# Performance work log

Hardware: AMD Instinct MI355X
Metric: run time of the kernel (lower is better)

Reference implementation:

```python
import jax, jax.numpy as jnp
import numpy as np

B, L = 16, 512          # samples x tokens-per-sample
S = B * L               # total packed tokens
H, HKV, D = 16, 4, 128  # query heads, kv heads, head_dim
G = H // HKV            # GQA group size
HID = 2048
EPS = 1e-6


def rmsnorm(x, w):
    # Qwen2RMSNorm: fp32 variance, scale by weight
    v = jnp.mean(x.astype(jnp.float32) ** 2, axis=-1, keepdims=True)
    return (x.astype(jnp.float32) * jax.lax.rsqrt(v + EPS)).astype(x.dtype) * w


def rotate_half(x):
    x1, x2 = jnp.split(x, 2, axis=-1)
    return jnp.concatenate([-x2, x1], axis=-1)


def setup_inputs() -> dict:
    key = jax.random.key(0)
    ks = jax.random.split(key, 24)
    f = lambda k, shp, s=0.02: (jax.random.normal(k, shp, dtype=jnp.float32) * s)
    inp = {
        'packed_sequence_und': f(ks[0], (S // 2, HID), 1.0),
        'packed_sequence_gen': f(ks[1], (S // 2, HID), 1.0),
        # und tokens on even slots, gen on odd slots -> irregular scatter
        'packed_und_token_indexes': jnp.arange(0, S, 2, dtype=jnp.int32),
        'packed_gen_token_indexes': jnp.arange(1, S, 2, dtype=jnp.int32),
        # und-path projections (q/k/v have bias, o does not)
        'q_w': f(ks[2], (H * D, HID)), 'q_b': f(ks[3], (H * D,)),
        'k_w': f(ks[4], (HKV * D, HID)), 'k_b': f(ks[5], (HKV * D,)),
        'v_w': f(ks[6], (HKV * D, HID)), 'v_b': f(ks[7], (HKV * D,)),
        'o_w': f(ks[8], (HID, H * D)),
        # gen-path (moe_gen) projections
        'q_w_g': f(ks[9], (H * D, HID)), 'q_b_g': f(ks[10], (H * D,)),
        'k_w_g': f(ks[11], (HKV * D, HID)), 'k_b_g': f(ks[12], (HKV * D,)),
        'v_w_g': f(ks[13], (HKV * D, HID)), 'v_b_g': f(ks[14], (HKV * D,)),
        'o_w_g': f(ks[15], (HID, H * D)),
        # qk-norm weights
        'qn_w': jnp.ones((D,), jnp.float32), 'kn_w': jnp.ones((D,), jnp.float32),
        'qn_w_g': jnp.ones((D,), jnp.float32), 'kn_w_g': jnp.ones((D,), jnp.float32),
    }
    # RoPE cos/sin for packed positions (position resets per sample)
    pos = jnp.tile(jnp.arange(L, dtype=jnp.float32), B)            # [S]
    inv_freq = 1.0 / (1e6 ** (jnp.arange(0, D, 2, dtype=jnp.float32) / D))
    freqs = pos[:, None] * inv_freq[None, :]                       # [S, D/2]
    emb = jnp.concatenate([freqs, freqs], axis=-1)                 # [S, D]
    inp['packed_cos'] = jnp.cos(emb)
    inp['packed_sin'] = jnp.sin(emb)
    return inp


def reference(packed_sequence_und, packed_sequence_gen, packed_cos, packed_sin,
              packed_und_token_indexes, packed_gen_token_indexes,
              q_w, q_b, k_w, k_b, v_w, v_b, o_w,
              q_w_g, q_b_g, k_w_g, k_b_g, v_w_g, v_b_g, o_w_g,
              qn_w, kn_w, qn_w_g, kn_w_g):
    ui, gi = packed_und_token_indexes, packed_gen_token_indexes
    # dual-path QKV projection + index scatter into shared packed buffers
    q = jnp.zeros((S, H * D), jnp.float32)
    q = q.at[ui].set(packed_sequence_und @ q_w.T + q_b)
    q = q.at[gi].set(packed_sequence_gen @ q_w_g.T + q_b_g)
    k = jnp.zeros((S, HKV * D), jnp.float32)
    k = k.at[ui].set(packed_sequence_und @ k_w.T + k_b)
    k = k.at[gi].set(packed_sequence_gen @ k_w_g.T + k_b_g)
    v = jnp.zeros((S, HKV * D), jnp.float32)
    v = v.at[ui].set(packed_sequence_und @ v_w.T + v_b)
    v = v.at[gi].set(packed_sequence_gen @ v_w_g.T + v_b_g)

    q = q.reshape(S, H, D)
    k = k.reshape(S, HKV, D)
    v = v.reshape(S, HKV, D)

    # per-stream QK RMSNorm, scattered back
    q = jnp.zeros_like(q).at[ui].set(rmsnorm(q[ui], qn_w)).at[gi].set(rmsnorm(q[gi], qn_w_g))
    k = jnp.zeros_like(k).at[ui].set(rmsnorm(k[ui], kn_w)).at[gi].set(rmsnorm(k[gi], kn_w_g))

    # RoPE (unsqueeze_dim=1)
    cos, sin = packed_cos[:, None, :], packed_sin[:, None, :]
    q = q * cos + rotate_half(q) * sin
    k = k * cos + rotate_half(k) * sin

    # block-diagonal causal attention over packed samples (GQA)
    qb_ = q.reshape(B, L, HKV, G, D)
    kb_ = k.reshape(B, L, HKV, D)
    vb_ = v.reshape(B, L, HKV, D)
    scale = 1.0 / np.sqrt(D)
    scores = jnp.einsum('bqhgd,bkhd->bhgqk', qb_, kb_) * scale   # [B,HKV,G,L,L]
    causal = jnp.tril(jnp.ones((L, L), bool))
    scores = jnp.where(causal, scores, -jnp.inf)
    probs = jax.nn.softmax(scores, axis=-1)
    out = jnp.einsum('bhgqk,bkhd->bqhgd', probs, vb_)            # [B,L,HKV,G,D]
    out = out.reshape(S, H * D)

    out_und = out[ui] @ o_w.T
    out_gen = out[gi] @ o_w_g.T
    return (out_und, out_gen)
```

## Files before the change

### kernel.cpp

```cpp
#include <hip/hip_runtime.h>

typedef __bf16 bf16;
typedef __bf16 bf16x8 __attribute__((ext_vector_type(8)));
typedef float  f32x4  __attribute__((ext_vector_type(4)));

#define HALF   4096
#define S_TOT  8192
#define HID    2048
#define NH     16
#define NKV    4
#define DH     128
#define LSEQ   512

typedef const __attribute__((address_space(1))) void* as1_cvp;
typedef __attribute__((address_space(3))) void* as3_vp;

__device__ __forceinline__ void gl2lds16(const void* g, void* l) {
    __builtin_amdgcn_global_load_lds((as1_cvp)g, (as3_vp)l, 16, 0, 0);
}

#define VMCNT(n) asm volatile("s_waitcnt vmcnt(" #n ")" ::: "memory")

struct CvtArgs {
    const float* src[10];
    bf16*        dst[10];
    int          n4[10];
};
__global__ __launch_bounds__(256) void k_convert_seg(CvtArgs a) {
    int rem = blockIdx.x;
    const float* src; bf16* dst;
    if      (rem < 8192)           { src=a.src[0]; dst=a.dst[0]; }
    else if ((rem -= 8192) < 8192) { src=a.src[1]; dst=a.dst[1]; }
    else if ((rem -= 8192) < 4096) { src=a.src[2]; dst=a.dst[2]; }
    else if ((rem -= 4096) < 1024) { src=a.src[3]; dst=a.dst[3]; }
    else if ((rem -= 1024) < 1024) { src=a.src[4]; dst=a.dst[4]; }
    else if ((rem -= 1024) < 4096) { src=a.src[5]; dst=a.dst[5]; }
    else if ((rem -= 4096) < 1024) { src=a.src[6]; dst=a.dst[6]; }
    else if ((rem -= 1024) < 1024) { src=a.src[7]; dst=a.dst[7]; }
    else if ((rem -= 1024) < 4096) { src=a.src[8]; dst=a.dst[8]; }
    else    { rem -= 4096;           src=a.src[9]; dst=a.dst[9]; }
    const int i = (rem << 8) + threadIdx.x;
    float4 v = ((const float4*)src)[i];
    union { bf16 b[4]; ushort4 u; } t;
    t.b[0] = (bf16)v.x; t.b[1] = (bf16)v.y; t.b[2] = (bf16)v.z; t.b[3] = (bf16)v.w;
    ((ushort4*)dst)[i] = t.u;
}

__global__ void k_invtyp(const int* __restrict__ ui, const int* __restrict__ gi,
                         int* __restrict__ it) {
    int t = blockIdx.x * 256 + threadIdx.x;
    if (t < HALF) { it[ui[t]] = t << 1; it[gi[t]] = (t << 1) | 1; }
}

__global__ __launch_bounds__(256) void k_gemm_qkv(
    const bf16* __restrict__ Xu, const bf16* __restrict__ Xg,
    const bf16* __restrict__ Wu, const bf16* __restrict__ Wg,
    const float* __restrict__ qbu, const float* __restrict__ kbu, const float* __restrict__ vbu,
    const float* __restrict__ qbg, const float* __restrict__ kbg, const float* __restrict__ vbg,
    const int* __restrict__ ui, const int* __restrict__ gi,
    bf16* __restrict__ qo, bf16* __restrict__ ko, bf16* __restrict__ vo)
{
    const int gen = blockIdx.z;
    const bf16* X = gen ? Xg : Xu;
    const bf16* W = gen ? Wg : Wu;
    const float* qb = gen ? qbg : qbu;
    const float* kb = gen ? kbg : kbu;
    const float* vb = gen ? vbg : vbu;
    const int* idx = gen ? gi : ui;

    __shared__ __align__(16) bf16 sA[128*32];
    __shared__ __align__(16) bf16 sB[128*32];

    const int tid = threadIdx.x;
    const int wave = tid >> 6, lane = tid & 63;
    const int lm = lane & 15, kq = lane >> 4;
    const int wm = wave >> 1, wn = wave & 1;
    const int m0 = blockIdx.y * 128, n0 = blockIdx.x * 128;

    f32x4 acc[4][4] = {};

    for (int k0 = 0; k0 < HID; k0 += 32) {
        __syncthreads();
        #pragma unroll
        for (int i = 0; i < 2; ++i) {
            const int g = i*4 + wave;
            const int c = g*64 + lane;
            const int row = c >> 2, col = c & 3;
            gl2lds16(X + (size_t)(m0+row)*HID + k0 + col*8, (char*)sA + (size_t)g*1024);
            gl2lds16(W + (size_t)(n0+row)*HID + k0 + col*8, (char*)sB + (size_t)g*1024);
        }
        __syncthreads();
        bf16x8 a[4], b[4];
        #pragma unroll
        for (int i = 0; i < 4; ++i) a[i] = *(const bf16x8*)&sA[(wm*64 + i*16 + lm)*32 + kq*8];
        #pragma unroll
        for (int j = 0; j < 4; ++j) b[j] = *(const bf16x8*)&sB[(wn*64 + j*16 + lm)*32 + kq*8];
        #pragma unroll
        for (int i = 0; i < 4; ++i)
            #pragma unroll
            for (int j = 0; j < 4; ++j)
                acc[i][j] = __builtin_amdgcn_mfma_f32_16x16x32_bf16(a[i], b[j], acc[i][j], 0, 0, 0);
    }

    #pragma unroll
    for (int i = 0; i < 4; ++i) {
        int srow[4];
        #pragma unroll
        for (int r = 0; r < 4; ++r) srow[r] = idx[m0 + wm*64 + i*16 + kq*4 + r];
        #pragma unroll
        for (int j = 0; j < 4; ++j) {
            const int o = n0 + wn*64 + j*16 + lm;
            bf16* dst; float bias; int off0, ld;
            if (o < 2048)      { dst = qo; ld = 2048; off0 = o;        bias = qb[o]; }
            else if (o < 2560) { dst = ko; ld = 512;  off0 = o - 2048; bias = kb[o-2048]; }
            else               { dst = vo; ld = 512;  off0 = o - 2560; bias = vb[o-2560]; }
            #pragma unroll
            for (int r = 0; r < 4; ++r)
                dst[(size_t)srow[r]*ld + off0] = (bf16)(acc[i][j][r] + bias);
        }
    }
}

#define C0 0
#define C1 16384
#define C2 32768
#define C3 49152

#define STG2(MB, KC, DST)                                                       \
    gl2lds16((MB) + (KC) + go0, (DST) + wave*1024);                             \
    gl2lds16((MB) + (KC) + go1, (DST) + 8192 + wave*1024);

#define PH(RD, MH, DOB, STG, TAIL)                                              \
  {                                                                             \
    _Pragma("unroll")                                                           \
    for (int im = 0; im < 4; ++im)                                              \
        a_[im] = *(const bf16x8*)(sAb + (RD) + (MH)*4096 + im*1024 + abase);    \
    if (DOB) {                                                                  \
        _Pragma("unroll")                                                       \
        for (int jn = 0; jn < 4; ++jn)                                          \
            b_[jn] = *(const bf16x8*)(sBb + (RD) + jn*1024 + bbase);            \
    }                                                                           \
    STG;                                                                        \
    __builtin_amdgcn_s_barrier();                                               \
    __builtin_amdgcn_s_setprio(1);                                              \
    _Pragma("unroll")                                                           \
    for (int im = 0; im < 4; ++im)                                              \
      _Pragma("unroll")                                                         \
      for (int jn = 0; jn < 4; ++jn)                                            \
        acc[(MH)*4+im][jn] = __builtin_amdgcn_mfma_f32_16x16x32_bf16(           \
            a_[im], b_[jn], acc[(MH)*4+im][jn], 0, 0, 0);                       \
    __builtin_amdgcn_s_setprio(0);                                              \
    TAIL;                                                                       \
    __builtin_amdgcn_s_barrier();                                               \
  }

__device__ __forceinline__ void gemm256_core(
    const bf16* __restrict__ A, const bf16* __restrict__ B,
    int m0, int n0, int tid, char* sAb, char* sBb, f32x4 (&acc)[8][4])
{
    const int lane = tid & 63;
    const int lm = lane & 15, kq = lane >> 4;
    const int wave = tid >> 6;
    const int wm = wave >> 2, wn = wave & 3;

    const int swz16 = (kq ^ ((lm >> 1) & 3)) * 16;
    const int abase = wm*8192 + lm*64 + swz16;
    const int bbase = wn*4096 + lm*64 + swz16;

    int go0, go1;
    {
        const int s0 = tid,        r0 = s0 >> 2, c0 = (s0 & 3) ^ ((r0 >> 1) & 3);
        const int s1 = 512 + tid,  r1 = s1 >> 2, c1 = (s1 & 3) ^ ((r1 >> 1) & 3);
        go0 = r0*HID + c0*8;
        go1 = r1*HID + c1*8;
    }
    const bf16* Ab = A + (size_t)m0*HID;
    const bf16* Bb = B + (size_t)n0*HID;

    bf16x8 a_[4], b_[4];

    STG2(Ab, 0,  sAb + C0);  STG2(Ab, 32, sAb + C1);
    STG2(Bb, 0,  sBb + C0);  STG2(Bb, 32, sBb + C1);
    STG2(Ab, 64, sAb + C2);  STG2(Bb, 64, sBb + C2);
    VMCNT(4);
    __builtin_amdgcn_s_barrier();

    #pragma unroll 1
    for (int i = 0; i < 15; ++i) {
        const int kc = 128*i;
        PH(C0, 0, 1, STG2(Ab, kc+96,  sAb+C3), (void)0);
        PH(C0, 1, 0, STG2(Bb, kc+96,  sBb+C3), (void)0);
        PH(C1, 0, 1, STG2(Ab, kc+128, sAb+C0), (void)0);
        PH(C1, 1, 0, STG2(Bb, kc+128, sBb+C0), VMCNT(4));
        PH(C2, 0, 1, STG2(Ab, kc+160, sAb+C1), (void)0);
        PH(C2, 1, 0, STG2(Bb, kc+160, sBb+C1), (void)0);
        PH(C3, 0, 1, STG2(Ab, kc+192, sAb+C2), (void)0);
        PH(C3, 1, 0, STG2(Bb, kc+192, sBb+C2), VMCNT(4));
    }
    {
        PH(C0, 0, 1, STG2(Ab, 2016, sAb+C3), (void)0);
        PH(C0, 1, 0, STG2(Bb, 2016, sBb+C3), (void)0);
        PH(C1, 0, 1, (void)0, (void)0);
        PH(C1, 1, 0, (void)0, VMCNT(0));
        PH(C2, 0, 1, (void)0, (void)0);
        PH(C2, 1, 0, (void)0, (void)0);
        PH(C3, 0, 1, (void)0, (void)0);
        PH(C3, 1, 0, (void)0, (void)0);
    }
}

__global__ __launch_bounds__(256) void k_norm_rope(
    bf16* __restrict__ qbuf, bf16* __restrict__ kbuf,
    const float* __restrict__ cosb, const float* __restrict__ sinb,
    const int* __restrict__ invtyp,
    const float* __restrict__ qnu, const float* __restrict__ qng,
    const float* __restrict__ knu, const float* __restrict__ kng)
{
    const int row = blockIdx.x * 4 + (threadIdx.x >> 6);
    const int lane = threadIdx.x & 63;
    const int s = row / (NH + NKV), hh = row % (NH + NKV);
    const int isg = invtyp[s] & 1;
    bf16* ptr; const float* w; float qs;
    if (hh < NH) { ptr = qbuf + (size_t)s*HID + hh*DH;           w = isg ? qng : qnu;
                   qs = 0.08838834764831845f * 1.4426950408889634f; }
    else         { ptr = kbuf + (size_t)s*(NKV*DH) + (hh-NH)*DH; w = isg ? kng : knu;
                   qs = 1.0f; }

    const unsigned u = *(const unsigned*)((const unsigned short*)ptr + 2*lane);
    const float f0 = __uint_as_float(u << 16);
    const float f1 = __uint_as_float(u & 0xffff0000u);
    float ss = f0*f0 + f1*f1;
    #pragma unroll
    for (int m = 32; m; m >>= 1) ss += __shfl_xor(ss, m, 64);
    const float r = rsqrtf(ss * (1.0f/128.0f) + 1e-6f);
    const float2 wv = *(const float2*)(w + 2*lane);
    const float xn0 = f0 * r * wv.x;
    const float xn1 = f1 * r * wv.y;
    const float po0 = __shfl_xor(xn0, 32, 64);
    const float po1 = __shfl_xor(xn1, 32, 64);
    const float2 c2 = *(const float2*)(cosb + (size_t)s*DH + 2*lane);
    const float2 s2 = *(const float2*)(sinb + (size_t)s*DH + 2*lane);
    const float sg = (lane < 32) ? -1.0f : 1.0f;
    const float o0 = (xn0 * c2.x + sg * po0 * s2.x) * qs;
    const float o1 = (xn1 * c2.y + sg * po1 * s2.y) * qs;
    union { unsigned short us[2]; unsigned u; } t;
    bf16 b0 = (bf16)o0, b1 = (bf16)o1;
    t.us[0] = *(unsigned short*)&b0; t.us[1] = *(unsigned short*)&b1;
    *(unsigned*)((unsigned short*)ptr + 2*lane) = t.u;
}

__global__ __launch_bounds__(256) void k_vtrans(const bf16* __restrict__ v, bf16* __restrict__ vt)
{
    __shared__ __align__(16) bf16 sT[64 * 132];
    const int kvh = blockIdx.y;
    const int s0 = blockIdx.x * 64;
    const int b = s0 >> 9;
    const int pos0 = s0 & 511;
    const int tid = threadIdx.x;

    #pragma unroll
    for (int i = 0; i < 4; ++i) {
        const int c = i*256 + tid;
        const int rowi = c >> 4, col8 = c & 15;
        const uint4 d = *(const uint4*)(v + (size_t)(s0 + rowi)*(NKV*DH) + kvh*DH + col8*8);
        uint2* lp = (uint2*)&sT[rowi*132 + col8*8];
        lp[0] = make_uint2(d.x, d.y);
        lp[1] = make_uint2(d.z, d.w);
    }
    __syncthreads();
    const int dd = tid >> 1, half = tid & 1;
    __align__(16) bf16 tmp[32];
    #pragma unroll
    for (int p = 0; p < 32; ++p) tmp[p] = sT[(half*32 + p)*132 + dd];
    bf16* dst = vt + ((size_t)(b*NKV + kvh)*DH + dd)*LSEQ + pos0 + half*32;
    #pragma unroll
    for (int q = 0; q < 8; ++q) ((ushort4*)dst)[q] = ((ushort4*)tmp)[q];
}

__global__ __launch_bounds__(256) void k_attn(
    const bf16* __restrict__ qbuf, const bf16* __restrict__ kbuf,
    const bf16* __restrict__ vt, const int* __restrict__ invtyp,
    bf16* __restrict__ aop_u, bf16* __restrict__ aop_g)
{
    __shared__ __align__(16) bf16 sK[2][64*128];
    __shared__ __align__(16) bf16 sV[2][128*64];
    __shared__ __align__(16) bf16 sP[4][16*72];

    const int pr = blockIdx.x;
    const int h = blockIdx.y, b = blockIdx.z;
    const int kvh = h >> 2;
    const int tid = threadIdx.x, wave = tid >> 6, lane = tid & 63;
    const int lm = lane & 15, kq = lane >> 4;

    const bf16* kbase = kbuf + ((size_t)(b*LSEQ))*(NKV*DH) + kvh*DH;
    const bf16* vbase = vt + ((size_t)(b*NKV + kvh)*DH)*LSEQ;
    bf16* const sPw = &sP[wave][0];

    #pragma unroll 1
    for (int t = 0; t < 2; ++t) {
        const int qt = t ? pr : 7 - pr;
        const int q0 = qt * 64;

        bf16x8 qfrag[4];
        {
            const bf16* qp = qbuf + ((size_t)(b*LSEQ + q0 + wave*16 + lm))*HID + h*DH;
            #pragma unroll
            for (int ks = 0; ks < 4; ++ks)
                qfrag[ks] = *(const bf16x8*)(qp + ks*32 + kq*8);
        }

        f32x4 accO[8] = {};
        float lpart[4] = {0.f, 0.f, 0.f, 0.f};

        if (t) __syncthreads();

        {
            const bf16* kp = kbase;
            const bf16* vp = vbase;
            #pragma unroll
            for (int i = 0; i < 4; ++i) {
                const int g = i*4 + wave;
                const int ch = g*64 + lane;
                { const int row = ch >> 4, cp = ch & 15;
                  const int c = (cp & 8) | ((cp ^ row) & 7);
                  gl2lds16(kp + (size_t)row*(NKV*DH) + c*8, (char*)&sK[0][0] + (size_t)g*1024); }
                { const int d = ch >> 3, cp = ch & 7;
                  const int c = (cp ^ d) & 7;
                  gl2lds16(vp + (size_t)d*LSEQ + c*8, (char*)&sV[0][0] + (size_t)g*1024); }
            }
        }

        for (int kt = 0; kt <= qt; ++kt) {
            const int cur = kt & 1;
            __syncthreads();

            if (kt < qt) {
                const bf16* kp = kbase + (size_t)((kt+1)*64)*(NKV*DH);
                const bf16* vp = vbase + (kt+1)*64;
                const int nxt = cur ^ 1;
                #pragma unroll
                for (int i = 0; i < 4; ++i) {
                    const int g = i*4 + wave;
                    const int ch = g*64 + lane;
                    { const int row = ch >> 4, cp = ch & 15;
                      const int c = (cp & 8) | ((cp ^ row) & 7);
                      gl2lds16(kp + (size_t)row*(NKV*DH) + c*8, (char*)&sK[nxt][0] + (size_t)g*1024); }
                    { const int d = ch >> 3, cp = ch & 7;
                      const int c = (cp ^ d) & 7;
                      gl2lds16(vp + (size_t)d*LSEQ + c*8, (char*)&sV[nxt][0] + (size_t)g*1024); }
                }
            }

            f32x4 s4[4] = {};
            #pragma unroll
            for (int ks = 0; ks < 4; ++ks) {
                const int cq = ks*4 + kq;
                const int cs = (cq & 8) | ((cq ^ lm) & 7);
                #pragma unroll
                for (int nt = 0; nt < 4; ++nt) {
                    bf16x8 bk = *(const bf16x8*)&sK[cur][(nt*16 + lm)*128 + cs*8];
                    s4[nt] = __builtin_amdgcn_mfma_f32_16x16x32_bf16(qfrag[ks], bk, s4[nt], 0, 0, 0);
                }
            }

            const bool diag = (kt == qt);
            #pragma unroll
            for (int r = 0; r < 4; ++r) {
                const int rloc = wave*16 + kq*4 + r;
                float v0 = s4[0][r], v1 = s4[1][r], v2 = s4[2][r], v3 = s4[3][r];
                if (diag) {
                    if (lm      > rloc) v0 = -1e30f;
                    if (lm + 16 > rloc) v1 = -1e30f;
                    if (lm + 32 > rloc) v2 = -1e30f;
                    if (lm + 48 > rloc) v3 = -1e30f;
                }
                const float p0 = exp2f(v0);
                const float p1 = exp2f(v1);
                const float p2 = exp2f(v2);
                const float p3 = exp2f(v3);
                lpart[r] += (p0 + p1) + (p2 + p3);
                const int prow = (kq*4 + r) * 72;
                sPw[prow + lm]      = (bf16)p0;
                sPw[prow + 16 + lm] = (bf16)p1;
                sPw[prow + 32 + lm] = (bf16)p2;
                sPw[prow + 48 + lm] = (bf16)p3;
            }

            #pragma unroll
            for (int pc = 0; pc < 2; ++pc) {
                bf16x8 ap = *(const bf16x8*)&sPw[lm*72 + pc*32 + kq*8];
                #pragma unroll
                for (int dt = 0; dt < 8; ++dt) {
                    const int cv = (pc*4 + kq);
                    const int cs = (cv ^ lm) & 7;
                    bf16x8 bv = *(const bf16x8*)&sV[cur][(dt*16 + lm)*64 + cs*8];
                    accO[dt] = __builtin_amdgcn_mfma_f32_16x16x32_bf16(ap, bv, accO[dt], 0, 0, 0);
                }
            }
        }

        #pragma unroll
        for (int r = 0; r < 4; ++r) {
            float l = lpart[r];
            l += __shfl_xor(l, 1, 64);
            l += __shfl_xor(l, 2, 64);
            l += __shfl_xor(l, 4, 64);
            l += __shfl_xor(l, 8, 64);
            const int srow = b*LSEQ + q0 + wave*16 + kq*4 + r;
            const int code = invtyp[srow];
            bf16* dst = (code & 1) ? aop_g : aop_u;
            const size_t off = (size_t)(code >> 1)*HID + h*DH;
            const float inv_l = 1.0f / l;
            #pragma unroll
            for (int dt = 0; dt < 8; ++dt)
                dst[off + dt*16 + lm] = (bf16)(accO[dt][r] * inv_l);
        }
    }
}

__global__ __launch_bounds__(512, 2) void k_gemm_out(
    const bf16* __restrict__ Au, const bf16* __restrict__ Ag,
    const bf16* __restrict__ Wu, const bf16* __restrict__ Wg,
    float* __restrict__ out)
{
    __shared__ __align__(16) bf16 sA[4][256*32];
    __shared__ __align__(16) bf16 sB[4][256*32];

    const int lin = blockIdx.x;
    const int idx = (lin & 7) * 32 + (lin >> 3);
    const int gen = idx / 128;
    const int rem = idx - gen * 128;
    const int my  = rem >> 3;
    const int nx_ = rem & 7;
    const int m0 = my * 256, n0 = nx_ * 256;

    const bf16* A = gen ? Ag : Au;
    const bf16* W = gen ? Wg : Wu;
    float* O = out + (size_t)gen * HALF * HID;

    const int tid = threadIdx.x;
    const int wave = tid >> 6, lane = tid & 63;
    const int lm = lane & 15, kq = lane >> 4;
    const int wm = wave >> 2, wn = wave & 3;

    f32x4 acc[8][4] = {};
    gemm256_core(A, W, m0, n0, tid, (char*)&sA[0][0], (char*)&sB[0][0], acc);

    #pragma unroll
    for (int im = 0; im < 8; ++im)
        #pragma unroll
        for (int jn = 0; jn < 4; ++jn)
            #pragma unroll
            for (int r = 0; r < 4; ++r)
                O[(size_t)(m0 + wm*128 + im*16 + kq*4 + r)*HID + (n0 + wn*64 + jn*16 + lm)]
                    = acc[im][jn][r];
}

extern "C" void kernel_launch(void* const* d_in, const int* in_sizes, int n_in,
                              void* d_out, int out_size, void* d_ws, size_t ws_size,
                              hipStream_t stream)
{
    (void)in_sizes; (void)n_in; (void)out_size; (void)ws_size;
    const float* x_u  = (const float*)d_in[0];
    const float* x_g  = (const float*)d_in[1];
    const int*   ui   = (const int*)d_in[2];
    const int*   gi   = (const int*)d_in[3];
    const float* q_w  = (const float*)d_in[4];
    const float* q_b  = (const float*)d_in[5];
    const float* k_w  = (const float*)d_in[6];
    const float* k_b  = (const float*)d_in[7];
    const float* v_w  = (const float*)d_in[8];
    const float* v_b  = (const float*)d_in[9];
    const float* o_w  = (const float*)d_in[10];
    const float* q_wg = (const float*)d_in[11];
    const float* q_bg = (const float*)d_in[12];
    const float* k_wg = (const float*)d_in[13];
    const float* k_bg = (const float*)d_in[14];
    const float* v_wg = (const float*)d_in[15];
    const float* v_bg = (const float*)d_in[16];
    const float* o_wg = (const float*)d_in[17];
    const float* qn_u = (const float*)d_in[18];
    const float* kn_u = (const float*)d_in[19];
    const float* qn_g = (const float*)d_in[20];
    const float* kn_g = (const float*)d_in[21];
    const float* cosb = (const float*)d_in[22];
    const float* sinb = (const float*)d_in[23];

    char* w = (char*)d_ws;
    auto alloc = [&](size_t bytes) { char* p = w; w += (bytes + 255) & ~(size_t)255; return p; };
    bf16* xb_u   = (bf16*)alloc((size_t)HALF*HID*2);
    bf16* xb_g   = (bf16*)alloc((size_t)HALF*HID*2);
    bf16* wqkv_u = (bf16*)alloc((size_t)3072*HID*2);
    bf16* wqkv_g = (bf16*)alloc((size_t)3072*HID*2);
    bf16* wo_u   = (bf16*)alloc((size_t)HID*HID*2);
    bf16* wo_g   = (bf16*)alloc((size_t)HID*HID*2);
    bf16* qbuf   = (bf16*)alloc((size_t)S_TOT*HID*2);
    bf16* kbuf   = (bf16*)alloc((size_t)S_TOT*NKV*DH*2);
    bf16* vbuf   = (bf16*)alloc((size_t)S_TOT*NKV*DH*2);
    bf16* vtb    = (bf16*)alloc((size_t)S_TOT*NKV*DH*2);
    int*  invtyp = (int*)alloc((size_t)S_TOT*4);
    bf16* aop_u = xb_u;
    bf16* aop_g = xb_g;

    CvtArgs ca;
    int si = 0;
    auto seg = [&](const float* s, bf16* d, size_t n) {
        ca.src[si] = s; ca.dst[si] = d; ca.n4[si] = (int)(n / 4); ++si;
    };
    seg(x_u,  xb_u,                (size_t)HALF*HID);
    seg(x_g,  xb_g,                (size_t)HALF*HID);
    seg(q_w,  wqkv_u,              (size_t)2048*HID);
    seg(k_w,  wqkv_u + 2048*HID,   (size_t)512*HID);
    seg(v_w,  wqkv_u + 2560*HID,   (size_t)512*HID);
    seg(q_wg, wqkv_g,              (size_t)2048*HID);
    seg(k_wg, wqkv_g + 2048*HID,   (size_t)512*HID);
    seg(v_wg, wqkv_g + 2560*HID,   (size_t)512*HID);
    seg(o_w,  wo_u,                (size_t)HID*HID);
    seg(o_wg, wo_g,                (size_t)HID*HID);
    k_convert_seg<<<36864, 256, 0, stream>>>(ca);

    k_invtyp<<<16, 256, 0, stream>>>(ui, gi, invtyp);

    k_gemm_qkv<<<dim3(24, 32, 2), 256, 0, stream>>>(
        xb_u, xb_g, wqkv_u, wqkv_g,
        q_b, k_b, v_b, q_bg, k_bg, v_bg,
        ui, gi, qbuf, kbuf, vbuf);

    k_norm_rope<<<(S_TOT*(NH+NKV))/4, 256, 0, stream>>>(
        qbuf, kbuf, cosb, sinb, invtyp, qn_u, qn_g, kn_u, kn_g);

    k_vtrans<<<dim3(S_TOT/64, NKV), 256, 0, stream>>>(vbuf, vtb);

    k_attn<<<dim3(4, NH, 16), 256, 0, stream>>>(
        qbuf, kbuf, vtb, invtyp, aop_u, aop_g);

    k_gemm_out<<<dim3(256), 512, 0, stream>>>(
        aop_u, aop_g, wo_u, wo_g, (float*)d_out);
}
```

Measured before the change: 504.9 us.

## Fuse QK RMSNorm and RoPE into QKV GEMM epilogue, merge invtyp into convert

The QKV projection epilogue now stages each 128-column head tile in shared memory, computes the per-row RMSNorm and RoPE there, and writes the final Q/K directly, so the separate norm/rope kernel and its read-modify-write pass over Q/K are gone. V tiles keep the plain bias-add scatter. The inverse-index kernel is folded into extra blocks of the convert launch, which saves one launch. In exchange the GEMM uses about 33KB more LDS, which may reduce occupancy, and the epilogue gains a barrier plus shuffle traffic.

```diff
diff --git a/kernel.cpp b/kernel.cpp
--- a/kernel.cpp
+++ b/kernel.cpp
@@ -21,13 +21,22 @@
 
 #define VMCNT(n) asm volatile("s_waitcnt vmcnt(" #n ")" ::: "memory")
 
+__device__ __forceinline__ float bfu_lo(unsigned u) { return __uint_as_float(u << 16); }
+__device__ __forceinline__ float bfu_hi(unsigned u) { return __uint_as_float(u & 0xffff0000u); }
+
 struct CvtArgs {
     const float* src[10];
     bf16*        dst[10];
     int          n4[10];
 };
-__global__ __launch_bounds__(256) void k_convert_seg(CvtArgs a) {
+__global__ __launch_bounds__(256) void k_convert_seg(CvtArgs a,
+    const int* __restrict__ ui, const int* __restrict__ gi, int* __restrict__ it) {
     int rem = blockIdx.x;
+    if (rem >= 36864) {
+        int t = (rem - 36864) * 256 + threadIdx.x;
+        if (t < HALF) { it[ui[t]] = t << 1; it[gi[t]] = (t << 1) | 1; }
+        return;
+    }
     const float* src; bf16* dst;
     if      (rem < 8192)           { src=a.src[0]; dst=a.dst[0]; }
     else if ((rem -= 8192) < 8192) { src=a.src[1]; dst=a.dst[1]; }
@@ -46,18 +55,15 @@
     ((ushort4*)dst)[i] = t.u;
 }
 
-__global__ void k_invtyp(const int* __restrict__ ui, const int* __restrict__ gi,
-                         int* __restrict__ it) {
-    int t = blockIdx.x * 256 + threadIdx.x;
-    if (t < HALF) { it[ui[t]] = t << 1; it[gi[t]] = (t << 1) | 1; }
-}
-
 __global__ __launch_bounds__(256) void k_gemm_qkv(
     const bf16* __restrict__ Xu, const bf16* __restrict__ Xg,
     const bf16* __restrict__ Wu, const bf16* __restrict__ Wg,
     const float* __restrict__ qbu, const float* __restrict__ kbu, const float* __restrict__ vbu,
     const float* __restrict__ qbg, const float* __restrict__ kbg, const float* __restrict__ vbg,
     const int* __restrict__ ui, const int* __restrict__ gi,
+    const float* __restrict__ qnu, const float* __restrict__ qng,
+    const float* __restrict__ knu, const float* __restrict__ kng,
+    const float* __restrict__ cosb, const float* __restrict__ sinb,
     bf16* __restrict__ qo, bf16* __restrict__ ko, bf16* __restrict__ vo)
 {
     const int gen = blockIdx.z;
@@ -70,6 +76,7 @@
 
     __shared__ __align__(16) bf16 sA[128*32];
     __shared__ __align__(16) bf16 sB[128*32];
+    __shared__ __align__(8)  bf16 sX[128*132];
 
     const int tid = threadIdx.x;
     const int wave = tid >> 6, lane = tid & 63;
@@ -102,21 +109,93 @@
                 acc[i][j] = __builtin_amdgcn_mfma_f32_16x16x32_bf16(a[i], b[j], acc[i][j], 0, 0, 0);
     }
 
+    const int nb = n0 >> 7;
+    if (nb >= 20) {
+        #pragma unroll
+        for (int i = 0; i < 4; ++i) {
+            int srow[4];
+            #pragma unroll
+            for (int r = 0; r < 4; ++r) srow[r] = idx[m0 + wm*64 + i*16 + kq*4 + r];
+            #pragma unroll
+            for (int j = 0; j < 4; ++j) {
+                const int o = n0 + wn*64 + j*16 + lm - 2560;
+                const float bias = vb[o];
+                #pragma unroll
+                for (int r = 0; r < 4; ++r)
+                    vo[(size_t)srow[r]*512 + o] = (bf16)(acc[i][j][r] + bias);
+            }
+        }
+        return;
+    }
+
+    const bool isQ = nb < 16;
+    const float* bptr = isQ ? (qb + n0) : (kb + (n0 - 2048));
+    const float* wnp  = isQ ? (gen ? qng : qnu) : (gen ? kng : knu);
+    bf16* obuf = isQ ? qo : ko;
+    const int old_ = isQ ? 2048 : 512;
+    const int ocol = (isQ ? nb : nb - 16) * 128;
+    const float qs = isQ ? (0.08838834764831845f * 1.4426950408889634f) : 1.0f;
+    char* const sXb = (char*)sX;
+
     #pragma unroll
-    for (int i = 0; i < 4; ++i) {
-        int srow[4];
-        #pragma unroll
-        for (int r = 0; r < 4; ++r) srow[r] = idx[m0 + wm*64 + i*16 + kq*4 + r];
+    for (int i = 0; i < 4; ++i)
         #pragma unroll
         for (int j = 0; j < 4; ++j) {
-            const int o = n0 + wn*64 + j*16 + lm;
-            bf16* dst; float bias; int off0, ld;
-            if (o < 2048)      { dst = qo; ld = 2048; off0 = o;        bias = qb[o]; }
-            else if (o < 2560) { dst = ko; ld = 512;  off0 = o - 2048; bias = kb[o-2048]; }
-            else               { dst = vo; ld = 512;  off0 = o - 2560; bias = vb[o-2560]; }
-            #pragma unroll
-            for (int r = 0; r < 4; ++r)
-                dst[(size_t)srow[r]*ld + off0] = (bf16)(acc[i][j][r] + bias);
+            const int d = wn*64 + j*16 + lm;
+            const float bias = bptr[d];
+            #pragma unroll
+            for (int r = 0; r < 4; ++r) {
+                bf16 xb = (bf16)(acc[i][j][r] + bias);
+                int us = (int)*(unsigned short*)&xb;
+                int pp = (us & 0xffff) | (__shfl_xor(us, 1, 64) << 16);
+                if (!(lm & 1)) {
+                    const int row = wm*64 + i*16 + kq*4 + r;
+                    *(unsigned*)(sXb + row*264 + d*2) = (unsigned)pp;
+                }
+            }
+        }
+    __syncthreads();
+
+    {
+        const int row = tid >> 1, hf = tid & 1;
+        const int srow = idx[m0 + row];
+        const char* rp = sXb + row*264;
+
+        float ss = 0.f;
+        #pragma unroll
+        for (int c = 0; c < 16; ++c) {
+            uint2 u2 = *(const uint2*)(rp + hf*128 + c*8);
+            float f0 = bfu_lo(u2.x), f1 = bfu_hi(u2.x);
+            float f2 = bfu_lo(u2.y), f3 = bfu_hi(u2.y);
+            ss += (f0*f0 + f1*f1) + (f2*f2 + f3*f3);
+        }
+        ss += __shfl_xor(ss, 1, 64);
+        const float rr = rsqrtf(ss * (1.0f/128.0f) + 1e-6f);
+
+        bf16* orow = obuf + (size_t)srow*old_ + ocol + hf*64;
+        const float* cz = cosb + (size_t)srow*DH + hf*64;
+        const float* sz = sinb + (size_t)srow*DH + hf*64;
+        const float sg = hf ? 1.0f : -1.0f;
+
+        #pragma unroll
+        for (int c = 0; c < 16; ++c) {
+            uint2 m2 = *(const uint2*)(rp + hf*128 + c*8);
+            uint2 o2 = *(const uint2*)(rp + (hf^1)*128 + c*8);
+            float4 wm4 = *(const float4*)(wnp + hf*64 + c*4);
+            float4 wo4 = *(const float4*)(wnp + (hf^1)*64 + c*4);
+            float4 c4  = *(const float4*)(cz + c*4);
+            float4 s4v = *(const float4*)(sz + c*4);
+            float xm0 = bfu_lo(m2.x)*rr, xm1 = bfu_hi(m2.x)*rr;
+            float xm2 = bfu_lo(m2.y)*rr, xm3 = bfu_hi(m2.y)*rr;
+            float xo0 = bfu_lo(o2.x)*rr, xo1 = bfu_hi(o2.x)*rr;
+            float xo2 = bfu_lo(o2.y)*rr, xo3 = bfu_hi(o2.y)*rr;
+            float r0 = (xm0*wm4.x*c4.x + sg*xo0*wo4.x*s4v.x) * qs;
+            float r1 = (xm1*wm4.y*c4.y + sg*xo1*wo4.y*s4v.y) * qs;
+            float r2 = (xm2*wm4.z*c4.z + sg*xo2*wo4.z*s4v.z) * qs;
+            float r3 = (xm3*wm4.w*c4.w + sg*xo3*wo4.w*s4v.w) * qs;
+            union { bf16 b[4]; ushort4 u; } t;
+            t.b[0] = (bf16)r0; t.b[1] = (bf16)r1; t.b[2] = (bf16)r2; t.b[3] = (bf16)r3;
+            *(ushort4*)(orow + c*4) = t.u;
         }
     }
 }
@@ -207,46 +286,6 @@
         PH(C3, 0, 1, (void)0, (void)0);
         PH(C3, 1, 0, (void)0, (void)0);
     }
-}
-
-__global__ __launch_bounds__(256) void k_norm_rope(
-    bf16* __restrict__ qbuf, bf16* __restrict__ kbuf,
-    const float* __restrict__ cosb, const float* __restrict__ sinb,
-    const int* __restrict__ invtyp,
-    const float* __restrict__ qnu, const float* __restrict__ qng,
-    const float* __restrict__ knu, const float* __restrict__ kng)
-{
-    const int row = blockIdx.x * 4 + (threadIdx.x >> 6);
-    const int lane = threadIdx.x & 63;
-    const int s = row / (NH + NKV), hh = row % (NH + NKV);
-    const int isg = invtyp[s] & 1;
-    bf16* ptr; const float* w; float qs;
-    if (hh < NH) { ptr = qbuf + (size_t)s*HID + hh*DH;           w = isg ? qng : qnu;
-                   qs = 0.08838834764831845f * 1.4426950408889634f; }
-    else         { ptr = kbuf + (size_t)s*(NKV*DH) + (hh-NH)*DH; w = isg ? kng : knu;
-                   qs = 1.0f; }
-
-    const unsigned u = *(const unsigned*)((const unsigned short*)ptr + 2*lane);
-    const float f0 = __uint_as_float(u << 16);
-    const float f1 = __uint_as_float(u & 0xffff0000u);
-    float ss = f0*f0 + f1*f1;
-    #pragma unroll
-    for (int m = 32; m; m >>= 1) ss += __shfl_xor(ss, m, 64);
-    const float r = rsqrtf(ss * (1.0f/128.0f) + 1e-6f);
-    const float2 wv = *(const float2*)(w + 2*lane);
-    const float xn0 = f0 * r * wv.x;
-    const float xn1 = f1 * r * wv.y;
-    const float po0 = __shfl_xor(xn0, 32, 64);
-    const float po1 = __shfl_xor(xn1, 32, 64);
-    const float2 c2 = *(const float2*)(cosb + (size_t)s*DH + 2*lane);
-    const float2 s2 = *(const float2*)(sinb + (size_t)s*DH + 2*lane);
-    const float sg = (lane < 32) ? -1.0f : 1.0f;
-    const float o0 = (xn0 * c2.x + sg * po0 * s2.x) * qs;
-    const float o1 = (xn1 * c2.y + sg * po1 * s2.y) * qs;
-    union { unsigned short us[2]; unsigned u; } t;
-    bf16 b0 = (bf16)o0, b1 = (bf16)o1;
-    t.us[0] = *(unsigned short*)&b0; t.us[1] = *(unsigned short*)&b1;
-    *(unsigned*)((unsigned short*)ptr + 2*lane) = t.u;
 }
 
 __global__ __launch_bounds__(256) void k_vtrans(const bf16* __restrict__ v, bf16* __restrict__ vt)
@@ -517,17 +556,13 @@
     seg(v_wg, wqkv_g + 2560*HID,   (size_t)512*HID);
     seg(o_w,  wo_u,                (size_t)HID*HID);
     seg(o_wg, wo_g,                (size_t)HID*HID);
-    k_convert_seg<<<36864, 256, 0, stream>>>(ca);
-
-    k_invtyp<<<16, 256, 0, stream>>>(ui, gi, invtyp);
+    k_convert_seg<<<36880, 256, 0, stream>>>(ca, ui, gi, invtyp);
 
     k_gemm_qkv<<<dim3(24, 32, 2), 256, 0, stream>>>(
         xb_u, xb_g, wqkv_u, wqkv_g,
         q_b, k_b, v_b, q_bg, k_bg, v_bg,
-        ui, gi, qbuf, kbuf, vbuf);
-
-    k_norm_rope<<<(S_TOT*(NH+NKV))/4, 256, 0, stream>>>(
-        qbuf, kbuf, cosb, sinb, invtyp, qn_u, qn_g, kn_u, kn_g);
+        ui, gi, qn_u, qn_g, kn_u, kn_g, cosb, sinb,
+        qbuf, kbuf, vbuf);
 
     k_vtrans<<<dim3(S_TOT/64, NKV), 256, 0, stream>>>(vbuf, vtb);
 
```

Measured after the change: 526.9 us. +4.4%, slower.
